# Performance work log

Measured on AMD Instinct MI355X. Metric: run time of the kernel, lower is better.

The kernel has to match this reference:

```python
import jax, jax.numpy as jnp
import numpy as np

N = 100000       # nodes
E = 3200000      # edges (before self-loops)
F_IN = 256       # input feature dim
HID = 32         # GCNConv output dim
CLASSES = 10


def setup_inputs() -> dict:
    key = jax.random.key(0)
    k1, k2, k3, k4 = jax.random.split(key, 4)
    feature = jax.random.normal(k1, (N, F_IN), dtype=jnp.float32)
    edge_index = jax.random.randint(k2, (2, E), 0, N, dtype=jnp.int64)
    W1 = jax.random.normal(k3, (F_IN, HID), dtype=jnp.float32) * (1.0 / np.sqrt(F_IN))
    b1 = jnp.zeros((HID,), dtype=jnp.float32)
    W2 = jax.random.normal(k4, (HID, CLASSES), dtype=jnp.float32) * (1.0 / np.sqrt(HID))
    b2 = jnp.zeros((CLASSES,), dtype=jnp.float32)
    return {"feature": feature, "edge_index": edge_index,
            "W1": W1, "b1": b1, "W2": W2, "b2": b2}


def reference(feature, edge_index, W1, b1, W2, b2):
    # --- GCNConv(features, 32): PyG semantics ---
    # add self-loops
    loops = jnp.arange(N, dtype=edge_index.dtype)
    row = jnp.concatenate([edge_index[0], loops])   # source nodes
    col = jnp.concatenate([edge_index[1], loops])   # target nodes
    # linear transform before propagation
    h = feature @ W1                                # [N, HID]
    # symmetric deg^{-1/2} normalization (degree counted at targets)
    deg = jax.ops.segment_sum(jnp.ones_like(col, dtype=h.dtype), col,
                              num_segments=N)       # [N], >=1 due to self-loops
    dinv = jax.lax.rsqrt(deg)
    norm = dinv[row] * dinv[col]                    # [E+N]
    # gather-scale-scatter aggregation
    msg = h[row] * norm[:, None]                    # [E+N, HID]
    agg = jax.ops.segment_sum(msg, col, num_segments=N) + b1  # [N, HID]
    # --- relu, (dropout: identity in eval), final linear, log_softmax ---
    act = jax.nn.relu(agg)
    logits = act @ W2 + b2                          # [N, CLASSES]
    return jax.nn.log_softmax(logits, axis=1)
```

## Files before the change

kernel.cpp:

```cpp
#include <hip/hip_runtime.h>
#include <hip/hip_fp16.h>

constexpr int N_NODES = 100000;
constexpr int E_EDGES = 3200000;
constexpr int F_IN    = 256;
constexpr int HID     = 32;
constexpr int NCLS    = 10;

constexpr int BUCK_SHIFT = 7;
constexpr int NPB        = 128;
constexpr int NBUCK      = (N_NODES + NPB - 1) / NPB;
constexpr int EPB        = 8192;
constexpr int NBLK1      = (E_EDGES + EPB - 1) / EPB;
constexpr int CAP        = 6144;

constexpr size_t OFF_FLAG = 0;
constexpr size_t OFF_GCUR = 4u << 10;
constexpr size_t OFF_BB   = 8u << 10;
constexpr size_t OFF_W1F  = 32u << 10;
constexpr size_t OFF_CNT  = 4u << 20;
constexpr size_t OFF_OFF  = 5u << 20;
constexpr size_t OFF_DINV = 6u << 20;
constexpr size_t OFF_CSR  = 7u << 20;
constexpr size_t OFF_BIN  = 20u << 20;
constexpr size_t OFF_HS   = 20u << 20;

typedef __attribute__((ext_vector_type(8))) short bf16x8;
typedef __attribute__((ext_vector_type(4))) float f32x4;

__device__ __forceinline__ unsigned pack_bf16x2(float a, float b) {
    unsigned ua = __float_as_uint(a), ub = __float_as_uint(b);
    ua = (ua + 0x7FFFu + ((ua >> 16) & 1u)) >> 16;
    ub = (ub + 0x7FFFu + ((ub >> 16) & 1u)) >> 16;
    return ua | (ub << 16);
}
__device__ __forceinline__ __half2 u2h(unsigned u) {
    union { unsigned u; __half2 h; } v; v.u = u; return v.h;
}

__device__ __forceinline__ int load_idx(const void* ei, long long i, int is64) {
    if (is64) return (int)((const long long*)ei)[i];
    return ((const int*)ei)[i];
}

__global__ __launch_bounds__(1024) void k_initw(const int* __restrict__ ei32,
                                                int* __restrict__ flag,
                                                int* __restrict__ gcur,
                                                const float* __restrict__ W1,
                                                unsigned* __restrict__ w1f) {
    __shared__ int nz;
    int tid = threadIdx.x;
    if (tid == 0) nz = 0;
    __syncthreads();
    if (ei32[2 * tid + 1] != 0) atomicOr(&nz, 1);
    __syncthreads();
    if (tid == 0) flag[0] = (nz == 0) ? 1 : 0;
    if (tid < NBUCK) gcur[tid] = tid * CAP;

    #pragma unroll
    for (int q = 0; q < 4; q++) {
        int i = tid + q * 1024;
        int p    = i & 3;
        int lane = (i >> 2) & 63;
        int f    = i >> 8;
        int ks = f >> 1, t = f & 1;
        int kg = lane >> 4, col = lane & 15;
        int k0 = ks * 32 + kg * 8 + p * 2;
        float w0 = W1[k0 * HID + t * 16 + col];
        float w1 = W1[(k0 + 1) * HID + t * 16 + col];
        w1f[i] = pack_bf16x2(w0, w1);
    }
}

__global__ __launch_bounds__(1024) void k_scat(const void* __restrict__ ei,
                                               const int* __restrict__ flag,
                                               int* __restrict__ gcur,
                                               unsigned* __restrict__ binned) {
    __shared__ unsigned       sval[EPB];
    __shared__ unsigned short sbuck[EPB];
    __shared__ int h[NBUCK];
    __shared__ int cur[NBUCK];
    int tid = threadIdx.x, blk = blockIdx.x;
    for (int i = tid; i < NBUCK; i += 1024) h[i] = 0;
    __syncthreads();

    int is64 = flag[0];
    int base = blk * EPB;
    int nedge = min(EPB, E_EDGES - base);
    for (int k = tid; k < nedge; k += 1024) {
        int i = base + k;
        int r = load_idx(ei, i, is64);
        int c = load_idx(ei, (long long)E_EDGES + i, is64);
        int b = c >> BUCK_SHIFT;
        sval[k]  = ((unsigned)r << BUCK_SHIFT) | ((unsigned)c & (NPB - 1));
        sbuck[k] = (unsigned short)b;
        atomicAdd(&h[b], 1);
    }
    __syncthreads();

    for (int j = tid; j < NBUCK; j += 1024) {
        int c = h[j];
        cur[j] = (c > 0) ? atomicAdd(&gcur[j], c) : 0;
    }
    __syncthreads();

    for (int k = tid; k < nedge; k += 1024) {
        int d = atomicAdd(&cur[sbuck[k]], 1);
        binned[d] = sval[k];
    }
}

__global__ __launch_bounds__(1024) void k_bscan(const int* __restrict__ gcur,
                                                int* __restrict__ bucketBase) {
    __shared__ int s[1024];
    int tid = threadIdx.x;
    int v = (tid < NBUCK) ? (gcur[tid] - tid * CAP) : 0;
    s[tid] = v;
    __syncthreads();
    for (int d = 1; d < 1024; d <<= 1) {
        int t = (tid >= d) ? s[tid - d] : 0;
        __syncthreads();
        s[tid] += t;
        __syncthreads();
    }
    if (tid < NBUCK) bucketBase[tid] = s[tid] - v;
    if (tid == 1023) bucketBase[NBUCK] = s[1023];
}

__global__ __launch_bounds__(512) void k_p2(const unsigned* __restrict__ binned,
                                            const int* __restrict__ gcur,
                                            const int* __restrict__ bucketBase,
                                            int* __restrict__ cnt,
                                            int* __restrict__ off,
                                            float* __restrict__ dinv,
                                            int* __restrict__ csr) {
    __shared__ int lcnt[NPB], sc[NPB], lcur[NPB];
    int b = blockIdx.x, tid = threadIdx.x;
    int s = b * CAP, e = gcur[b];
    int db = bucketBase[b];
    if (tid < NPB) lcnt[tid] = 0;
    __syncthreads();
    for (int i = s + tid; i < e; i += 512)
        atomicAdd(&lcnt[binned[i] & (NPB - 1)], 1);
    __syncthreads();
    if (tid < NPB) sc[tid] = lcnt[tid];
    __syncthreads();
    for (int d = 1; d < NPB; d <<= 1) {
        int t = 0;
        if (tid < NPB && tid >= d) t = sc[tid - d];
        __syncthreads();
        if (tid < NPB) sc[tid] += t;
        __syncthreads();
    }
    if (tid < NPB) {
        int o = db + sc[tid] - lcnt[tid];
        lcur[tid] = o;
        int node = b * NPB + tid;
        if (node < N_NODES) {
            off[node]  = o;
            cnt[node]  = lcnt[tid];
            dinv[node] = rsqrtf((float)lcnt[tid] + 1.0f);
        }
    }
    __syncthreads();
    for (int i = s + tid; i < e; i += 512) {
        unsigned p = binned[i];
        int pos = atomicAdd(&lcur[p & (NPB - 1)], 1);
        csr[pos] = (int)(p >> BUCK_SHIFT);
    }
}

__global__ __launch_bounds__(256) void k_h(const float* __restrict__ feat,
                                           const unsigned* __restrict__ w1f,
                                           const float* __restrict__ dinv,
                                           unsigned short* __restrict__ hs16s) {
    int tid  = threadIdx.x;
    int lane = tid & 63;
    long wid = (long)blockIdx.x * 4 + (tid >> 6);
    int n0 = (int)(wid * 16);
    if (n0 >= N_NODES) return;

    bf16x8 bfrag[16];
    const bf16x8* wv = (const bf16x8*)w1f;
    #pragma unroll
    for (int f = 0; f < 16; f++) bfrag[f] = wv[f * 64 + lane];

    int arow = lane & 15;
    int kg   = lane >> 4;
    const float4* fr = (const float4*)(feat + (size_t)(n0 + arow) * F_IN);

    f32x4 acc0 = {0.f, 0.f, 0.f, 0.f};
    f32x4 acc1 = {0.f, 0.f, 0.f, 0.f};

    #pragma unroll
    for (int ks = 0; ks < 8; ks++) {
        float4 fa = fr[ks * 8 + kg * 2 + 0];
        float4 fb = fr[ks * 8 + kg * 2 + 1];
        unsigned au[4];
        au[0] = pack_bf16x2(fa.x, fa.y);
        au[1] = pack_bf16x2(fa.z, fa.w);
        au[2] = pack_bf16x2(fb.x, fb.y);
        au[3] = pack_bf16x2(fb.z, fb.w);
        bf16x8 af = *(bf16x8*)au;
        acc0 = __builtin_amdgcn_mfma_f32_16x16x32_bf16(af, bfrag[ks * 2 + 0], acc0, 0, 0, 0);
        acc1 = __builtin_amdgcn_mfma_f32_16x16x32_bf16(af, bfrag[ks * 2 + 1], acc1, 0, 0, 0);
    }

    int rb = kg * 4;
    #pragma unroll
    for (int r = 0; r < 4; r++) {
        int node = n0 + rb + r;
        float di = dinv[node];
        hs16s[(size_t)node * HID + arow]      = __half_as_ushort(__float2half(acc0[r] * di));
        hs16s[(size_t)node * HID + 16 + arow] = __half_as_ushort(__float2half(acc1[r] * di));
    }
}

__global__ __launch_bounds__(256) void k_aggout(const int* __restrict__ off,
                                                const int* __restrict__ cnt,
                                                const int* __restrict__ csr,
                                                const unsigned* __restrict__ hs16,
                                                const float* __restrict__ dinv,
                                                const float* __restrict__ b1,
                                                const float* __restrict__ W2,
                                                const float* __restrict__ b2,
                                                float* __restrict__ out) {
    __shared__ float W2s[HID * NCLS];
    __shared__ float b2s[NCLS];
    int tid = threadIdx.x;
    for (int i = tid; i < HID * NCLS; i += 256) W2s[i] = W2[i];
    if (tid < NCLS) b2s[tid] = b2[tid];
    __syncthreads();

    int l2   = tid & 3;
    int g    = tid >> 2;
    int node = blockIdx.x * 64 + g;
    if (node >= N_NODES) return;

    int o = off[node];
    int n = cnt[node];

    const uint4* hsv = (const uint4*)hs16;
    uint4 ps = hsv[(size_t)node * 4 + l2];
    __half2 s0 = u2h(ps.x), s1 = u2h(ps.y), s2 = u2h(ps.z), s3 = u2h(ps.w);

    #define ADDQ(Q) \
        s0 = __hadd2(s0, u2h(Q.x)); s1 = __hadd2(s1, u2h(Q.y)); \
        s2 = __hadd2(s2, u2h(Q.z)); s3 = __hadd2(s3, u2h(Q.w));

    int i = 0;
    for (; i + 8 <= n; i += 8) {
        int r0 = csr[o + i + 0];
        int r1 = csr[o + i + 1];
        int r2 = csr[o + i + 2];
        int r3 = csr[o + i + 3];
        int r4 = csr[o + i + 4];
        int r5 = csr[o + i + 5];
        int r6 = csr[o + i + 6];
        int r7 = csr[o + i + 7];
        uint4 q0 = hsv[(size_t)r0 * 4 + l2];
        uint4 q1 = hsv[(size_t)r1 * 4 + l2];
        uint4 q2 = hsv[(size_t)r2 * 4 + l2];
        uint4 q3 = hsv[(size_t)r3 * 4 + l2];
        uint4 q4 = hsv[(size_t)r4 * 4 + l2];
        uint4 q5 = hsv[(size_t)r5 * 4 + l2];
        uint4 q6 = hsv[(size_t)r6 * 4 + l2];
        uint4 q7 = hsv[(size_t)r7 * 4 + l2];
        ADDQ(q0) ADDQ(q1) ADDQ(q2) ADDQ(q3)
        ADDQ(q4) ADDQ(q5) ADDQ(q6) ADDQ(q7)
    }
    for (; i < n; i++) {
        uint4 q = hsv[(size_t)csr[o + i] * 4 + l2];
        ADDQ(q)
    }
    #undef ADDQ

    float2 f0 = __half22float2(s0);
    float2 f1 = __half22float2(s1);
    float2 f2 = __half22float2(s2);
    float2 f3 = __half22float2(s3);

    float di = dinv[node];
    float4 b1lo = *(const float4*)(b1 + 8 * l2);
    float4 b1hi = *(const float4*)(b1 + 8 * l2 + 4);
    float act[8];
    act[0] = fmaxf(b1lo.x + f0.x * di, 0.f);
    act[1] = fmaxf(b1lo.y + f0.y * di, 0.f);
    act[2] = fmaxf(b1lo.z + f1.x * di, 0.f);
    act[3] = fmaxf(b1lo.w + f1.y * di, 0.f);
    act[4] = fmaxf(b1hi.x + f2.x * di, 0.f);
    act[5] = fmaxf(b1hi.y + f2.y * di, 0.f);
    act[6] = fmaxf(b1hi.z + f3.x * di, 0.f);
    act[7] = fmaxf(b1hi.w + f3.y * di, 0.f);

    float p[NCLS];
    #pragma unroll
    for (int c = 0; c < NCLS; c++) {
        float s = 0.f;
        #pragma unroll
        for (int k = 0; k < 8; k++) s = fmaf(act[k], W2s[(8 * l2 + k) * NCLS + c], s);
        p[c] = s;
    }

    #pragma unroll
    for (int d = 1; d < 4; d <<= 1) {
        #pragma unroll
        for (int c = 0; c < NCLS; c++) p[c] += __shfl_xor(p[c], d, 4);
    }

    #pragma unroll
    for (int c = 0; c < NCLS; c++) p[c] += b2s[c];
    float m = p[0];
    #pragma unroll
    for (int c = 1; c < NCLS; c++) m = fmaxf(m, p[c]);
    float se = 0.f;
    #pragma unroll
    for (int c = 0; c < NCLS; c++) se += expf(p[c] - m);
    float lse = m + logf(se);

    #pragma unroll
    for (int q = 0; q < 3; q++) {
        int c = l2 + 4 * q;
        if (c < NCLS) {
            float v = p[0];
            #pragma unroll
            for (int cc = 1; cc < NCLS; cc++) v = (c == cc) ? p[cc] : v;
            out[(size_t)node * NCLS + c] = v - lse;
        }
    }
}

extern "C" void kernel_launch(void* const* d_in, const int* in_sizes, int n_in,
                              void* d_out, int out_size, void* d_ws, size_t ws_size,
                              hipStream_t stream) {
    const float* feat = (const float*)d_in[0];
    const void*  ei   = d_in[1];
    const float* W1   = (const float*)d_in[2];
    const float* b1   = (const float*)d_in[3];
    const float* W2   = (const float*)d_in[4];
    const float* b2   = (const float*)d_in[5];
    float* out = (float*)d_out;

    char* ws = (char*)d_ws;
    int*      flag   = (int*)(ws + OFF_FLAG);
    int*      gcur   = (int*)(ws + OFF_GCUR);
    int*      bbase  = (int*)(ws + OFF_BB);
    unsigned* w1f    = (unsigned*)(ws + OFF_W1F);
    int*      cnt    = (int*)(ws + OFF_CNT);
    int*      off    = (int*)(ws + OFF_OFF);
    float*    dinv   = (float*)(ws + OFF_DINV);
    int*      csr    = (int*)(ws + OFF_CSR);
    unsigned* binned = (unsigned*)(ws + OFF_BIN);
    unsigned* hs16   = (unsigned*)(ws + OFF_HS);

    k_initw<<<1, 1024, 0, stream>>>((const int*)ei, flag, gcur, W1, w1f);
    k_scat<<<NBLK1, 1024, 0, stream>>>(ei, flag, gcur, binned);
    k_bscan<<<1, 1024, 0, stream>>>(gcur, bbase);
    k_p2<<<NBUCK, 512, 0, stream>>>(binned, gcur, bbase, cnt, off, dinv, csr);

    k_h<<<(N_NODES / 16 + 3) / 4, 256, 0, stream>>>(feat, w1f, dinv,
                                                    (unsigned short*)hs16);
    k_aggout<<<(N_NODES + 63) / 64, 256, 0, stream>>>(off, cnt, csr, hs16, dinv,
                                                      b1, W2, b2, out);
}
```

Measured before the change: 122.8 us.

## Drop bucket scan kernel, use padded CSR offsets and stage bucket in LDS

```diff
diff --git a/kernel.cpp b/kernel.cpp
--- a/kernel.cpp
+++ b/kernel.cpp
@@ -16,14 +16,13 @@
 
 constexpr size_t OFF_FLAG = 0;
 constexpr size_t OFF_GCUR = 4u << 10;
-constexpr size_t OFF_BB   = 8u << 10;
 constexpr size_t OFF_W1F  = 32u << 10;
-constexpr size_t OFF_CNT  = 4u << 20;
-constexpr size_t OFF_OFF  = 5u << 20;
-constexpr size_t OFF_DINV = 6u << 20;
-constexpr size_t OFF_CSR  = 7u << 20;
-constexpr size_t OFF_BIN  = 20u << 20;
-constexpr size_t OFF_HS   = 20u << 20;
+constexpr size_t OFF_CNT  = 1u << 20;
+constexpr size_t OFF_OFF  = 3u << 20;
+constexpr size_t OFF_DINV = 4u << 20;
+constexpr size_t OFF_CSR  = 5u << 20;
+constexpr size_t OFF_BIN  = 25u << 20;
+constexpr size_t OFF_HS   = 25u << 20;
 
 typedef __attribute__((ext_vector_type(8))) short bf16x8;
 typedef __attribute__((ext_vector_type(4))) float f32x4;
@@ -110,38 +109,24 @@
     }
 }
 
-__global__ __launch_bounds__(1024) void k_bscan(const int* __restrict__ gcur,
-                                                int* __restrict__ bucketBase) {
-    __shared__ int s[1024];
-    int tid = threadIdx.x;
-    int v = (tid < NBUCK) ? (gcur[tid] - tid * CAP) : 0;
-    s[tid] = v;
-    __syncthreads();
-    for (int d = 1; d < 1024; d <<= 1) {
-        int t = (tid >= d) ? s[tid - d] : 0;
-        __syncthreads();
-        s[tid] += t;
-        __syncthreads();
-    }
-    if (tid < NBUCK) bucketBase[tid] = s[tid] - v;
-    if (tid == 1023) bucketBase[NBUCK] = s[1023];
-}
-
-__global__ __launch_bounds__(512) void k_p2(const unsigned* __restrict__ binned,
-                                            const int* __restrict__ gcur,
-                                            const int* __restrict__ bucketBase,
-                                            int* __restrict__ cnt,
-                                            int* __restrict__ off,
-                                            float* __restrict__ dinv,
-                                            int* __restrict__ csr) {
+__global__ __launch_bounds__(1024) void k_p2(const unsigned* __restrict__ binned,
+                                             const int* __restrict__ gcur,
+                                             int* __restrict__ cnt,
+                                             int* __restrict__ off,
+                                             float* __restrict__ dinv,
+                                             int* __restrict__ csr) {
+    __shared__ unsigned sval[CAP];
     __shared__ int lcnt[NPB], sc[NPB], lcur[NPB];
     int b = blockIdx.x, tid = threadIdx.x;
-    int s = b * CAP, e = gcur[b];
-    int db = bucketBase[b];
+    int s = b * CAP;
+    int m = gcur[b] - s;
     if (tid < NPB) lcnt[tid] = 0;
     __syncthreads();
-    for (int i = s + tid; i < e; i += 512)
-        atomicAdd(&lcnt[binned[i] & (NPB - 1)], 1);
+    for (int i = tid; i < m; i += 1024) {
+        unsigned p = binned[s + i];
+        sval[i] = p;
+        atomicAdd(&lcnt[p & (NPB - 1)], 1);
+    }
     __syncthreads();
     if (tid < NPB) sc[tid] = lcnt[tid];
     __syncthreads();
@@ -153,7 +138,7 @@
         __syncthreads();
     }
     if (tid < NPB) {
-        int o = db + sc[tid] - lcnt[tid];
+        int o = s + sc[tid] - lcnt[tid];
         lcur[tid] = o;
         int node = b * NPB + tid;
         if (node < N_NODES) {
@@ -163,8 +148,8 @@
         }
     }
     __syncthreads();
-    for (int i = s + tid; i < e; i += 512) {
-        unsigned p = binned[i];
+    for (int i = tid; i < m; i += 1024) {
+        unsigned p = sval[i];
         int pos = atomicAdd(&lcur[p & (NPB - 1)], 1);
         csr[pos] = (int)(p >> BUCK_SHIFT);
     }
@@ -344,7 +329,6 @@
     char* ws = (char*)d_ws;
     int*      flag   = (int*)(ws + OFF_FLAG);
     int*      gcur   = (int*)(ws + OFF_GCUR);
-    int*      bbase  = (int*)(ws + OFF_BB);
     unsigned* w1f    = (unsigned*)(ws + OFF_W1F);
     int*      cnt    = (int*)(ws + OFF_CNT);
     int*      off    = (int*)(ws + OFF_OFF);
@@ -355,8 +339,7 @@
 
     k_initw<<<1, 1024, 0, stream>>>((const int*)ei, flag, gcur, W1, w1f);
     k_scat<<<NBLK1, 1024, 0, stream>>>(ei, flag, gcur, binned);
-    k_bscan<<<1, 1024, 0, stream>>>(gcur, bbase);
-    k_p2<<<NBUCK, 512, 0, stream>>>(binned, gcur, bbase, cnt, off, dinv, csr);
+    k_p2<<<NBUCK, 1024, 0, stream>>>(binned, gcur, cnt, off, dinv, csr);
 
     k_h<<<(N_NODES / 16 + 3) / 4, 256, 0, stream>>>(feat, w1f, dinv,
                                                     (unsigned short*)hs16);
```

After: 119.6 us. 2.6% less time.
